# Performance work log

Hardware: AMD Instinct MI355X
Metric: run time of the kernel (lower is better)

Reference implementation:

```python
import jax, jax.numpy as jnp
import numpy as np

B, L, D, H = 2, 2048, 2048, 16
Dh = D // H
THETA = 500000.0


def _init_rope(dim, seq_len, n_heads):
    # Returns freqs_cis of shape (1, seq_len, 1, head_dim//2, 2) -> [..., 0]=cos, [..., 1]=sin
    hd = dim // n_heads
    inv_freqs = 1.0 / (THETA ** (jnp.arange(0, hd, 2, dtype=jnp.float32) / hd))
    t = jnp.arange(seq_len, dtype=jnp.float32)
    freqs = jnp.outer(t, inv_freqs).astype(jnp.float32)  # (L, hd/2)
    fc = jnp.stack([jnp.cos(freqs)[None, :, None, :],
                    jnp.sin(freqs)[None, :, None, :]], axis=3)  # (1, L, 1, 2, hd/2)
    return fc.transpose(0, 1, 2, 4, 3)  # (1, L, 1, hd/2, 2)


def _apply_rope(q, k, freqs_cis):
    def rotate(x):
        x2 = x.reshape(*x.shape[:-1], -1, 2)  # (B, L, H, Dh/2, 2)
        f = freqs_cis[:, :x.shape[1]]
        cos, sin = f[..., 0], f[..., 1]
        r = jnp.stack([x2[..., 0] * cos - x2[..., 1] * sin,
                       x2[..., 1] * cos + x2[..., 0] * sin], axis=-1)
        return r.reshape(*x.shape)
    return rotate(q), rotate(k)


def setup_inputs() -> dict:
    key = jax.random.key(0)
    kx, kq, kk, kv, ko = jax.random.split(key, 5)
    scale = 1.0 / np.sqrt(D)
    x = jax.random.normal(kx, (B, L, D), dtype=jnp.float32)
    Wq = jax.random.normal(kq, (D, H, Dh), dtype=jnp.float32) * scale
    Wk = jax.random.normal(kk, (D, H, Dh), dtype=jnp.float32) * scale
    Wv = jax.random.normal(kv, (D, H, Dh), dtype=jnp.float32) * scale
    Wo = jax.random.normal(ko, (D, D), dtype=jnp.float32) * scale
    return {"x": x, "Wq": Wq, "Wk": Wk, "Wv": Wv, "Wo": Wo}


def reference(x, Wq, Wk, Wv, Wo):
    freqs_cis = _init_rope(D, L, H)
    q = jnp.einsum('bld,dhk->blhk', x, Wq)  # (B, L, H, Dh)
    k = jnp.einsum('bld,dhk->blhk', x, Wk)
    v = jnp.einsum('bld,dhk->blhk', x, Wv)
    q, k = _apply_rope(q, k, freqs_cis)
    q = q / (Dh ** 0.5)
    att = jnp.einsum('bqhd,bkhd->bhqk', q, k)  # (B, H, L, L)
    Lq = x.shape[1]
    mask = jnp.tril(jnp.ones((1, 1, Lq, Lq), dtype=jnp.bool_))
    neg_inf = jnp.finfo(jnp.float32).min
    att = jnp.where(mask, att, neg_inf)
    att = jax.nn.softmax(att, axis=-1)
    out = jnp.einsum('bhqk,bkhd->bqhd', att, v)  # (B, L, H, Dh)
    out = out.reshape(x.shape)
    return jnp.einsum('bld,de->ble', out, Wo)
```

## Files before the change

### kernel.cpp

```cpp
#include <hip/hip_runtime.h>

typedef unsigned short u16;
typedef unsigned int u32;

#define Bb 2
#define Lc 2048
#define Dc 2048
#define Hc 16
#define DhC 128

typedef __bf16 bf16x8 __attribute__((ext_vector_type(8)));
typedef float f32x4 __attribute__((ext_vector_type(4)));
typedef float f32x16 __attribute__((ext_vector_type(16)));

__device__ __forceinline__ u16 f2b(float f) {
  u32 u = __float_as_uint(f);
  u32 r = (u + 0x7fffu + ((u >> 16) & 1u)) >> 16;
  return (u16)r;
}
__device__ __forceinline__ float b2f(u16 u) {
  return __uint_as_float(((u32)u) << 16);
}

__device__ __forceinline__ u32 cvtpk(float lo, float hi) {
  u32 r;
  asm("v_cvt_pk_bf16_f32 %0, %1, %2" : "=v"(r) : "v"(lo), "v"(hi));
  return r;
}

__device__ __forceinline__ void gll16(const void* g, void* l) {
  __builtin_amdgcn_global_load_lds(
      (const __attribute__((address_space(1))) u32*)g,
      (__attribute__((address_space(3))) u32*)l, 16, 0, 0);
}

__global__ __launch_bounds__(256) void sniff_dtype(const u16* __restrict__ x,
                                                   int* __restrict__ flag) {
  __shared__ int bad;
  if (threadIdx.x == 0) bad = 0;
  __syncthreads();
  int local = 0;
  for (int i = threadIdx.x; i < 65536; i += 256) {
    float v = fabsf(b2f(x[i]));
    if (!(v < 1000.f)) local = 1;
  }
  if (local) atomicOr(&bad, 1);
  __syncthreads();
  if (threadIdx.x == 0) *flag = bad;
}

__global__ __launch_bounds__(256) void conv_x(const void* __restrict__ in,
                                              u16* __restrict__ out,
                                              const int* __restrict__ flag) {
  const int f32 = *flag;
  const int i0 = (blockIdx.x * 256 + threadIdx.x) * 4;
  if (f32) {
    const float* p = (const float*)in;
#pragma unroll
    for (int j = 0; j < 4; j++) out[i0 + j] = f2b(p[i0 + j]);
  } else {
    const u16* p = (const u16*)in;
#pragma unroll
    for (int j = 0; j < 4; j++) out[i0 + j] = p[i0 + j];
  }
}

__global__ __launch_bounds__(256) void transpose2d_conv(const void* __restrict__ in,
                                                        u16* __restrict__ out,
                                                        const int* __restrict__ flag) {
  __shared__ __align__(16) u16 tile[64][65];
  const int f32 = *flag;
  const int r0 = blockIdx.y * 64, c0 = blockIdx.x * 64;
  const int tc = threadIdx.x & 63, tr4 = threadIdx.x >> 6;
#pragma unroll
  for (int p = 0; p < 16; p++) {
    int r = tr4 + p * 4;
    size_t idx = (size_t)(r0 + r) * 2048 + c0 + tc;
    tile[r][tc] = f32 ? f2b(((const float*)in)[idx]) : ((const u16*)in)[idx];
  }
  __syncthreads();
#pragma unroll
  for (int p = 0; p < 16; p++) {
    int rr = tr4 + p * 4;
    out[(size_t)(c0 + rr) * 2048 + r0 + tc] = tile[tc][rr];
  }
}

template <typename OutT>
__device__ __forceinline__ void gemmfo_core(const u16* __restrict__ A,
                                            const u16* __restrict__ Bt,
                                            OutT* __restrict__ C,
                                            int Ntiles, size_t bufStride) {
  constexpr int K = 2048;
  constexpr int NTK = K / 32;
  __shared__ __align__(16) u16 Als[4][128 * 32];
  __shared__ __align__(16) u16 Bls[4][256 * 32];

  const int tid = threadIdx.x;
  const int lane = tid & 63, w = tid >> 6;
  const int quad = lane >> 4, l15 = lane & 15;
  const int wm = w >> 2, wn = w & 3;

  const int nwg = 32 * Ntiles;
  const int q8 = nwg >> 3;
  const int id = (int)blockIdx.x;
  const int swz = (id & 7) * q8 + (id >> 3);
  const int m0 = (swz & 31) * 128;
  const int n0 = (swz >> 5) * 256;

  const int sc = (lane >> 4) * 8;
  const u16* aSrc = A + (size_t)(m0 + w * 16 + l15) * K + sc;
  const u16* bSrc0 = Bt + (size_t)(n0 + (2 * w) * 16 + l15) * K + sc;
  const u16* bSrc1 = Bt + (size_t)(n0 + (2 * w + 1) * 16 + l15) * K + sc;

  const f32x4 fz = {0.f, 0.f, 0.f, 0.f};
  f32x4 acc[4][4];
#pragma unroll
  for (int i = 0; i < 4; i++)
#pragma unroll
    for (int j = 0; j < 4; j++) acc[i][j] = fz;

  auto stage = [&](int t) {
    const int s = t & 3;
    const int k = t * 32;
    gll16(aSrc + k, &Als[s][w * 512]);
    gll16(bSrc0 + k, &Bls[s][(2 * w) * 512]);
    gll16(bSrc1 + k, &Bls[s][(2 * w + 1) * 512]);
  };

  auto compute = [&](int t) {
    const u16* abuf = Als[t & 3];
    const u16* bbuf = Bls[t & 3];
    bf16x8 afr[4], bfr[4];
#pragma unroll
    for (int mt = 0; mt < 4; mt++)
      afr[mt] = *(const bf16x8*)(&abuf[(wm * 4 + mt) * 512 + lane * 8]);
#pragma unroll
    for (int nt = 0; nt < 4; nt++)
      bfr[nt] = *(const bf16x8*)(&bbuf[(wn * 4 + nt) * 512 + lane * 8]);
    asm volatile("s_waitcnt lgkmcnt(0)" ::: "memory");
    __builtin_amdgcn_sched_barrier(0);
    __builtin_amdgcn_s_setprio(1);
#pragma unroll
    for (int mt = 0; mt < 4; mt++)
#pragma unroll
      for (int nt = 0; nt < 4; nt++)
        acc[mt][nt] = __builtin_amdgcn_mfma_f32_16x16x32_bf16(
            afr[mt], bfr[nt], acc[mt][nt], 0, 0, 0);
    __builtin_amdgcn_s_setprio(0);
  };

  stage(0); stage(1); stage(2);
  asm volatile("s_waitcnt vmcnt(6)" ::: "memory");
  __builtin_amdgcn_s_barrier();

  for (int t = 0; t < NTK - 3; ++t) {
    stage(t + 3);
    compute(t);
    asm volatile("s_waitcnt vmcnt(6)" ::: "memory");
    __builtin_amdgcn_s_barrier();
  }
  compute(NTK - 3);
  asm volatile("s_waitcnt vmcnt(3)" ::: "memory");
  __builtin_amdgcn_s_barrier();
  compute(NTK - 2);
  asm volatile("s_waitcnt vmcnt(0)" ::: "memory");
  __builtin_amdgcn_s_barrier();
  compute(NTK - 1);

#pragma unroll
  for (int mt = 0; mt < 4; mt++)
#pragma unroll
    for (int nt = 0; nt < 4; nt++) {
      const int colg = n0 + wn * 64 + nt * 16 + l15;
      const size_t cbase = (size_t)(colg >> 11) * bufStride + (colg & 2047);
#pragma unroll
      for (int r = 0; r < 4; r++) {
        const int row = m0 + wm * 64 + mt * 16 + quad * 4 + r;
        const float v = acc[mt][nt][r];
        if constexpr (sizeof(OutT) == 2)
          C[cbase + (size_t)row * 2048] = f2b(v);
        else
          C[cbase + (size_t)row * 2048] = v;
      }
    }
}

__global__ __launch_bounds__(512, 2) void gemmfo_bf(const u16* __restrict__ A,
                                                    const u16* __restrict__ Bt,
                                                    u16* __restrict__ C,
                                                    int Ntiles, size_t bufStride) {
  gemmfo_core<u16>(A, Bt, C, Ntiles, bufStride);
}
__global__ __launch_bounds__(512, 2) void gemmfo_f32(const u16* __restrict__ A,
                                                     const u16* __restrict__ Bt,
                                                     float* __restrict__ C,
                                                     int Ntiles, size_t bufStride) {
  gemmfo_core<float>(A, Bt, C, Ntiles, bufStride);
}

__global__ __launch_bounds__(256) void transpose_v_k(const u16* __restrict__ V,
                                                     u16* __restrict__ Vt) {
  __shared__ __align__(16) u16 tile[64][65];
  const int z = blockIdx.z;
  const int b = z >> 4, h = z & 15;
  const int l0 = blockIdx.y * 64, d0 = blockIdx.x * 64;
  const int tc = threadIdx.x & 63, tr4 = threadIdx.x >> 6;
#pragma unroll
  for (int p = 0; p < 16; p++) {
    int l = tr4 + p * 4;
    tile[l][tc] = V[(size_t)((b * Lc + l0 + l) * Hc + h) * DhC + d0 + tc];
  }
  __syncthreads();
#pragma unroll
  for (int p = 0; p < 16; p++) {
    int dd = tr4 + p * 4;
    Vt[((size_t)z * DhC + d0 + dd) * Lc + l0 + tc] = tile[tc][dd];
  }
}

__global__ __launch_bounds__(256) void rope_qk(u16* __restrict__ Q, u16* __restrict__ K) {
  const int idx = blockIdx.x * 256 + threadIdx.x;
  const int j = idx & 63;
  const int l = (idx >> 10) & 2047;
  const float inv = expf(-0.2050369278f * (float)j);
  const float ang = (float)l * inv;
  float s, c;
  sincosf(ang, &s, &c);
  const size_t off = (size_t)idx * 2;
  const float q0 = b2f(Q[off]), q1 = b2f(Q[off + 1]);
  const float k0 = b2f(K[off]), k1 = b2f(K[off + 1]);
  const float sc = 0.08838834764f;
  Q[off]     = f2b((q0 * c - q1 * s) * sc);
  Q[off + 1] = f2b((q1 * c + q0 * s) * sc);
  K[off]     = f2b(k0 * c - k1 * s);
  K[off + 1] = f2b(k1 * c + k0 * s);
}

#define NEGBIG (-3.0e30f)
__global__ __launch_bounds__(256, 2) void flash_attn(const u16* __restrict__ Q,
                                                     const u16* __restrict__ Kg,
                                                     const u16* __restrict__ Vt,
                                                     u16* __restrict__ O) {
  __shared__ __align__(16) u16 Ks[2][64 * 128];
  __shared__ __align__(16) u16 Vs[2][128 * 64];
  const int tid = threadIdx.x;
  const int lane = tid & 63, w = tid >> 6;
  const int l31 = lane & 31, hib = lane >> 5;
  const int bh = blockIdx.y;
  const int b = bh >> 4, h = bh & 15;
  const int qt = (bh & 16) ? (int)blockIdx.x : (15 - (int)blockIdx.x);
  const int q0 = qt * 128;
  const int qw0 = q0 + w * 32;
  const int nkv = 2 * qt + 2;

  const int krl = lane >> 4, ksl = lane & 15;
  const int vrl = lane >> 3, vsl = lane & 7;

  bf16x8 qf[8];
  {
    const u16* qptr = Q + ((size_t)(b * Lc + qw0 + l31) * Hc + h) * DhC + 8 * hib;
#pragma unroll
    for (int s = 0; s < 8; s++) qf[s] = *(const bf16x8*)(qptr + s * 16);
  }

  {
#pragma unroll
    for (int p = 0; p < 4; p++) {
      const int r = p * 16 + w * 4 + krl;
      const int c = ksl ^ (r & 15);
      gll16(Kg + ((size_t)(b * Lc + r) * Hc + h) * DhC + c * 8,
            &Ks[0][(p * 256 + w * 64) * 8]);
    }
#pragma unroll
    for (int p = 0; p < 4; p++) {
      const int r = p * 32 + w * 8 + vrl;
      const int c = vsl ^ (r & 7);
      gll16(Vt + ((size_t)bh * DhC + r) * Lc + c * 8,
            &Vs[0][(p * 256 + w * 64) * 8]);
    }
  }

  f32x16 o[4];
#pragma unroll
  for (int dt = 0; dt < 4; dt++) o[dt] = (f32x16)0.0f;
  float mrow = NEGBIG, lrow = 0.f;

  __syncthreads();

  for (int kvt = 0; kvt < nkv; kvt++) {
    const int cur = kvt & 1;
    const u16* Ksc = Ks[cur];
    const u16* Vsc = Vs[cur];

    if (kvt + 1 < nkv) {
      const int nv0 = (kvt + 1) * 64;
      const int nxt = cur ^ 1;
#pragma unroll
      for (int p = 0; p < 4; p++) {
        const int r = p * 16 + w * 4 + krl;
        const int c = ksl ^ (r & 15);
        gll16(Kg + ((size_t)(b * Lc + nv0 + r) * Hc + h) * DhC + c * 8,
              &Ks[nxt][(p * 256 + w * 64) * 8]);
      }
#pragma unroll
      for (int p = 0; p < 4; p++) {
        const int r = p * 32 + w * 8 + vrl;
        const int c = vsl ^ (r & 7);
        gll16(Vt + ((size_t)bh * DhC + r) * Lc + nv0 + c * 8,
              &Vs[nxt][(p * 256 + w * 64) * 8]);
      }
    }

    const int kv0 = kvt * 64;
    const bool active = (kv0 <= qw0 + 31);
    if (active) {
      f32x16 s0 = (f32x16)0.0f, s1 = (f32x16)0.0f;
      __builtin_amdgcn_s_setprio(1);
#pragma unroll
      for (int s = 0; s < 8; s++) {
        const int ch = ((2 * s + hib) ^ (l31 & 15)) * 8;
        bf16x8 k0 = *(const bf16x8*)(&Ksc[l31 * 128 + ch]);
        bf16x8 k1 = *(const bf16x8*)(&Ksc[(32 + l31) * 128 + ch]);
        s0 = __builtin_amdgcn_mfma_f32_32x32x16_bf16(k0, qf[s], s0, 0, 0, 0);
        s1 = __builtin_amdgcn_mfma_f32_32x32x16_bf16(k1, qf[s], s1, 0, 0, 0);
      }
      __builtin_amdgcn_s_setprio(0);

      if (kv0 + 63 > qw0) {
        const int qg = qw0 + l31;
#pragma unroll
        for (int r = 0; r < 16; r++) {
          const int cr = (r & 3) + 8 * (r >> 2) + 4 * hib;
          if (kv0 + cr > qg) s0[r] = NEGBIG;
          if (kv0 + 32 + cr > qg) s1[r] = NEGBIG;
        }
      }

      float mx;
      {
        float a[8];
#pragma unroll
        for (int i = 0; i < 8; i++)
          a[i] = fmaxf(fmaxf(s0[i], s0[i + 8]), fmaxf(s1[i], s1[i + 8]));
        float b0 = fmaxf(a[0], a[4]), b1 = fmaxf(a[1], a[5]);
        float b2 = fmaxf(a[2], a[6]), b3 = fmaxf(a[3], a[7]);
        mx = fmaxf(fmaxf(b0, b1), fmaxf(b2, b3));
      }
      mx = fmaxf(mx, __shfl_xor(mx, 32, 64));

      if (!__all(mx - mrow <= 8.f)) {
        const float mnew = fmaxf(mrow, mx);
        const float al = __expf(mrow - mnew);
#pragma unroll
        for (int dt = 0; dt < 4; dt++)
#pragma unroll
          for (int e = 0; e < 16; e++) o[dt][e] *= al;
        lrow *= al;
        mrow = mnew;
      }

#pragma unroll
      for (int i = 0; i < 16; i++) {
        s0[i] = __expf(s0[i] - mrow);
        s1[i] = __expf(s1[i] - mrow);
      }
      float sm;
      {
        float a[8];
#pragma unroll
        for (int i = 0; i < 8; i++)
          a[i] = (s0[i] + s0[i + 8]) + (s1[i] + s1[i + 8]);
        sm = ((a[0] + a[4]) + (a[1] + a[5])) + ((a[2] + a[6]) + (a[3] + a[7]));
      }
      sm += __shfl_xor(sm, 32, 64);
      lrow += sm;

      bf16x8 paf[4];
#pragma unroll
      for (int t = 0; t < 2; t++) {
#pragma unroll
        for (int h8 = 0; h8 < 2; h8++) {
          const int rB = 8 * h8;
          u32 lo0, lo1, hi0, hi1;
          if (t == 0) {
            lo0 = cvtpk(s0[rB + 0], s0[rB + 1]);
            lo1 = cvtpk(s0[rB + 2], s0[rB + 3]);
            hi0 = cvtpk(s0[rB + 4], s0[rB + 5]);
            hi1 = cvtpk(s0[rB + 6], s0[rB + 7]);
          } else {
            lo0 = cvtpk(s1[rB + 0], s1[rB + 1]);
            lo1 = cvtpk(s1[rB + 2], s1[rB + 3]);
            hi0 = cvtpk(s1[rB + 4], s1[rB + 5]);
            hi1 = cvtpk(s1[rB + 6], s1[rB + 7]);
          }
          const u32 g0 = hib ? lo0 : hi0;
          const u32 g1 = hib ? lo1 : hi1;
          const u32 r0 = (u32)__shfl_xor((int)g0, 32, 64);
          const u32 r1 = (u32)__shfl_xor((int)g1, 32, 64);
          union { u32 u[4]; bf16x8 v; } pu;
          pu.u[0] = hib ? r0 : lo0;
          pu.u[1] = hib ? r1 : lo1;
          pu.u[2] = hib ? hi0 : r0;
          pu.u[3] = hib ? hi1 : r1;
          paf[2 * t + h8] = pu.v;
        }
      }

      __builtin_amdgcn_s_setprio(1);
#pragma unroll
      for (int B = 0; B < 4; B++) {
#pragma unroll
        for (int dt = 0; dt < 4; dt++) {
          const bf16x8 vf = *(const bf16x8*)(
              &Vsc[(32 * dt + l31) * 64 + (((2 * B + hib) ^ (l31 & 7))) * 8]);
          o[dt] = __builtin_amdgcn_mfma_f32_32x32x16_bf16(paf[B], vf, o[dt], 0, 0, 0);
        }
      }
      __builtin_amdgcn_s_setprio(0);
    }

    __syncthreads();
  }

#pragma unroll
  for (int r = 0; r < 16; r++) {
    const int cr = (r & 3) + 8 * (r >> 2) + 4 * hib;
    const float linv = 1.0f / __shfl(lrow, cr, 64);
    const size_t rowoff = ((size_t)(b * Lc + qw0 + cr) * Hc + h) * DhC + l31;
#pragma unroll
    for (int dt = 0; dt < 4; dt++)
      O[rowoff + 32 * dt] = f2b(o[dt][r] * linv);
  }
}

extern "C" void kernel_launch(void* const* d_in, const int* in_sizes, int n_in,
                              void* d_out, int out_size, void* d_ws, size_t ws_size,
                              hipStream_t stream) {
  const void* x  = d_in[0];
  const void* Wq = d_in[1];
  const void* Wk = d_in[2];
  const void* Wv = d_in[3];
  const void* Wo = d_in[4];
  float* out = (float*)d_out;

  char* w = (char*)d_ws;
  const size_t WSZ = (size_t)2048 * 2048;
  const size_t XSZ = (size_t)Bb * Lc * Dc;
  int* flag = (int*)w;
  u16* WT  = (u16*)(w + 256);
  u16* xc  = WT + WSZ;
  u16* Qb  = xc + XSZ;
  u16* Kb  = Qb + XSZ;
  u16* Vb  = Kb + XSZ;
  u16* Vtb = xc;
  u16* Ob  = Vb;
  u16* WTall = (u16*)d_out;

  sniff_dtype<<<1, 256, 0, stream>>>((const u16*)x, flag);
  conv_x<<<(int)(XSZ / 1024), 256, 0, stream>>>(x, xc, flag);

  dim3 tgrid(32, 32);

  transpose2d_conv<<<tgrid, 256, 0, stream>>>(Wq, WTall, flag);
  transpose2d_conv<<<tgrid, 256, 0, stream>>>(Wk, WTall + WSZ, flag);
  transpose2d_conv<<<tgrid, 256, 0, stream>>>(Wv, WTall + 2 * WSZ, flag);

  gemmfo_bf<<<dim3(768), 512, 0, stream>>>(xc, WTall, Qb, 24, XSZ);

  rope_qk<<<(Bb * Lc * Hc * 64) / 256, 256, 0, stream>>>(Qb, Kb);

  dim3 vgrid(2, 32, 32);
  transpose_v_k<<<vgrid, 256, 0, stream>>>(Vb, Vtb);

  dim3 fgrid(16, 32);
  flash_attn<<<fgrid, 256, 0, stream>>>(Qb, Kb, Vtb, Ob);

  transpose2d_conv<<<tgrid, 256, 0, stream>>>(Wo, WT, flag);
  gemmfo_f32<<<dim3(256), 512, 0, stream>>>(Ob, WT, out, 8, 0);
}
```

Measured before the change: 614.3 us.

## Shrink GEMM tiles to 128x128, batch weight transposes, and share RoPE trig across batch

The projection GEMMs switch from 512-thread 128x256 tiles with 4-stage LDS buffering to 256-thread 128x128 tiles with 3-stage buffering and four blocks per CU, which doubles the grid and lowers per-block LDS. The three Q/K/V weight transposes merge into one launch. RoPE now computes sincos once per (l, h, j) and applies it to both batch elements, using exp2f. Smaller tiles give more blocks and better occupancy but less operand reuse per block, and a shallower prefetch pipeline.

```diff
diff --git a/kernel.cpp b/kernel.cpp
--- a/kernel.cpp
+++ b/kernel.cpp
@@ -65,11 +65,8 @@
   }
 }
 
-__global__ __launch_bounds__(256) void transpose2d_conv(const void* __restrict__ in,
-                                                        u16* __restrict__ out,
-                                                        const int* __restrict__ flag) {
+__device__ __forceinline__ void tconv_body(const void* in, u16* out, int f32) {
   __shared__ __align__(16) u16 tile[64][65];
-  const int f32 = *flag;
   const int r0 = blockIdx.y * 64, c0 = blockIdx.x * 64;
   const int tc = threadIdx.x & 63, tr4 = threadIdx.x >> 6;
 #pragma unroll
@@ -86,32 +83,48 @@
   }
 }
 
+__global__ __launch_bounds__(256) void transpose2d_conv(const void* __restrict__ in,
+                                                        u16* __restrict__ out,
+                                                        const int* __restrict__ flag) {
+  tconv_body(in, out, *flag);
+}
+
+__global__ __launch_bounds__(256) void transpose3_conv(const void* __restrict__ W0,
+                                                       const void* __restrict__ W1,
+                                                       const void* __restrict__ W2,
+                                                       u16* __restrict__ out,
+                                                       const int* __restrict__ flag) {
+  const int z = blockIdx.z;
+  const void* in = (z == 0) ? W0 : (z == 1) ? W1 : W2;
+  tconv_body(in, out + (size_t)z * 2048 * 2048, *flag);
+}
+
 template <typename OutT>
-__device__ __forceinline__ void gemmfo_core(const u16* __restrict__ A,
-                                            const u16* __restrict__ Bt,
-                                            OutT* __restrict__ C,
-                                            int Ntiles, size_t bufStride) {
+__device__ __forceinline__ void gemmp_core(const u16* __restrict__ A,
+                                           const u16* __restrict__ Bt,
+                                           OutT* __restrict__ C,
+                                           int Ntiles, size_t bufStride) {
   constexpr int K = 2048;
   constexpr int NTK = K / 32;
-  __shared__ __align__(16) u16 Als[4][128 * 32];
-  __shared__ __align__(16) u16 Bls[4][256 * 32];
+  __shared__ __align__(16) u16 Als[3][128 * 32];
+  __shared__ __align__(16) u16 Bls[3][128 * 32];
 
   const int tid = threadIdx.x;
   const int lane = tid & 63, w = tid >> 6;
   const int quad = lane >> 4, l15 = lane & 15;
-  const int wm = w >> 2, wn = w & 3;
+  const int wm = w >> 1, wn = w & 1;
 
   const int nwg = 32 * Ntiles;
   const int q8 = nwg >> 3;
   const int id = (int)blockIdx.x;
   const int swz = (id & 7) * q8 + (id >> 3);
   const int m0 = (swz & 31) * 128;
-  const int n0 = (swz >> 5) * 256;
-
-  const int sc = (lane >> 4) * 8;
-  const u16* aSrc = A + (size_t)(m0 + w * 16 + l15) * K + sc;
-  const u16* bSrc0 = Bt + (size_t)(n0 + (2 * w) * 16 + l15) * K + sc;
-  const u16* bSrc1 = Bt + (size_t)(n0 + (2 * w + 1) * 16 + l15) * K + sc;
+  const int n0 = (swz >> 5) * 128;
+
+  const u16* aSrc0 = A + (size_t)(m0 + (2 * w) * 16 + l15) * K + quad * 8;
+  const u16* aSrc1 = A + (size_t)(m0 + (2 * w + 1) * 16 + l15) * K + quad * 8;
+  const u16* bSrc0 = Bt + (size_t)(n0 + (2 * w) * 16 + l15) * K + quad * 8;
+  const u16* bSrc1 = Bt + (size_t)(n0 + (2 * w + 1) * 16 + l15) * K + quad * 8;
 
   const f32x4 fz = {0.f, 0.f, 0.f, 0.f};
   f32x4 acc[4][4];
@@ -121,23 +134,23 @@
     for (int j = 0; j < 4; j++) acc[i][j] = fz;
 
   auto stage = [&](int t) {
-    const int s = t & 3;
+    const int s = t % 3;
     const int k = t * 32;
-    gll16(aSrc + k, &Als[s][w * 512]);
+    gll16(aSrc0 + k, &Als[s][(2 * w) * 512]);
+    gll16(aSrc1 + k, &Als[s][(2 * w + 1) * 512]);
     gll16(bSrc0 + k, &Bls[s][(2 * w) * 512]);
     gll16(bSrc1 + k, &Bls[s][(2 * w + 1) * 512]);
   };
 
   auto compute = [&](int t) {
-    const u16* abuf = Als[t & 3];
-    const u16* bbuf = Bls[t & 3];
+    const int s = t % 3;
     bf16x8 afr[4], bfr[4];
 #pragma unroll
     for (int mt = 0; mt < 4; mt++)
-      afr[mt] = *(const bf16x8*)(&abuf[(wm * 4 + mt) * 512 + lane * 8]);
+      afr[mt] = *(const bf16x8*)(&Als[s][(wm * 4 + mt) * 512 + lane * 8]);
 #pragma unroll
     for (int nt = 0; nt < 4; nt++)
-      bfr[nt] = *(const bf16x8*)(&bbuf[(wn * 4 + nt) * 512 + lane * 8]);
+      bfr[nt] = *(const bf16x8*)(&Bls[s][(wn * 4 + nt) * 512 + lane * 8]);
     asm volatile("s_waitcnt lgkmcnt(0)" ::: "memory");
     __builtin_amdgcn_sched_barrier(0);
     __builtin_amdgcn_s_setprio(1);
@@ -150,19 +163,17 @@
     __builtin_amdgcn_s_setprio(0);
   };
 
-  stage(0); stage(1); stage(2);
-  asm volatile("s_waitcnt vmcnt(6)" ::: "memory");
+  stage(0);
+  stage(1);
+  asm volatile("s_waitcnt vmcnt(4)" ::: "memory");
   __builtin_amdgcn_s_barrier();
 
-  for (int t = 0; t < NTK - 3; ++t) {
-    stage(t + 3);
+  for (int t = 0; t < NTK - 2; ++t) {
+    stage(t + 2);
     compute(t);
-    asm volatile("s_waitcnt vmcnt(6)" ::: "memory");
+    asm volatile("s_waitcnt vmcnt(4)" ::: "memory");
     __builtin_amdgcn_s_barrier();
   }
-  compute(NTK - 3);
-  asm volatile("s_waitcnt vmcnt(3)" ::: "memory");
-  __builtin_amdgcn_s_barrier();
   compute(NTK - 2);
   asm volatile("s_waitcnt vmcnt(0)" ::: "memory");
   __builtin_amdgcn_s_barrier();
@@ -186,17 +197,17 @@
     }
 }
 
-__global__ __launch_bounds__(512, 2) void gemmfo_bf(const u16* __restrict__ A,
+__global__ __launch_bounds__(256, 4) void gemmp_bf(const u16* __restrict__ A,
+                                                   const u16* __restrict__ Bt,
+                                                   u16* __restrict__ C,
+                                                   int Ntiles, size_t bufStride) {
+  gemmp_core<u16>(A, Bt, C, Ntiles, bufStride);
+}
+__global__ __launch_bounds__(256, 4) void gemmp_f32(const u16* __restrict__ A,
                                                     const u16* __restrict__ Bt,
-                                                    u16* __restrict__ C,
+                                                    float* __restrict__ C,
                                                     int Ntiles, size_t bufStride) {
-  gemmfo_core<u16>(A, Bt, C, Ntiles, bufStride);
-}
-__global__ __launch_bounds__(512, 2) void gemmfo_f32(const u16* __restrict__ A,
-                                                     const u16* __restrict__ Bt,
-                                                     float* __restrict__ C,
-                                                     int Ntiles, size_t bufStride) {
-  gemmfo_core<float>(A, Bt, C, Ntiles, bufStride);
+  gemmp_core<float>(A, Bt, C, Ntiles, bufStride);
 }
 
 __global__ __launch_bounds__(256) void transpose_v_k(const u16* __restrict__ V,
@@ -222,19 +233,23 @@
 __global__ __launch_bounds__(256) void rope_qk(u16* __restrict__ Q, u16* __restrict__ K) {
   const int idx = blockIdx.x * 256 + threadIdx.x;
   const int j = idx & 63;
-  const int l = (idx >> 10) & 2047;
-  const float inv = expf(-0.2050369278f * (float)j);
+  const int h = (idx >> 6) & 15;
+  const int l = idx >> 10;
+  const float inv = exp2f(-0.2958057561f * (float)j);
   const float ang = (float)l * inv;
   float s, c;
   sincosf(ang, &s, &c);
-  const size_t off = (size_t)idx * 2;
-  const float q0 = b2f(Q[off]), q1 = b2f(Q[off + 1]);
-  const float k0 = b2f(K[off]), k1 = b2f(K[off + 1]);
   const float sc = 0.08838834764f;
-  Q[off]     = f2b((q0 * c - q1 * s) * sc);
-  Q[off + 1] = f2b((q1 * c + q0 * s) * sc);
-  K[off]     = f2b(k0 * c - k1 * s);
-  K[off + 1] = f2b(k1 * c + k0 * s);
+#pragma unroll
+  for (int b = 0; b < Bb; b++) {
+    const size_t off = ((size_t)((b * Lc + l) * Hc + h)) * DhC + 2 * j;
+    const float q0 = b2f(Q[off]), q1 = b2f(Q[off + 1]);
+    const float k0 = b2f(K[off]), k1 = b2f(K[off + 1]);
+    Q[off]     = f2b((q0 * c - q1 * s) * sc);
+    Q[off + 1] = f2b((q1 * c + q0 * s) * sc);
+    K[off]     = f2b(k0 * c - k1 * s);
+    K[off + 1] = f2b(k1 * c + k0 * s);
+  }
 }
 
 #define NEGBIG (-3.0e30f)
@@ -460,15 +475,11 @@
   sniff_dtype<<<1, 256, 0, stream>>>((const u16*)x, flag);
   conv_x<<<(int)(XSZ / 1024), 256, 0, stream>>>(x, xc, flag);
 
-  dim3 tgrid(32, 32);
-
-  transpose2d_conv<<<tgrid, 256, 0, stream>>>(Wq, WTall, flag);
-  transpose2d_conv<<<tgrid, 256, 0, stream>>>(Wk, WTall + WSZ, flag);
-  transpose2d_conv<<<tgrid, 256, 0, stream>>>(Wv, WTall + 2 * WSZ, flag);
-
-  gemmfo_bf<<<dim3(768), 512, 0, stream>>>(xc, WTall, Qb, 24, XSZ);
-
-  rope_qk<<<(Bb * Lc * Hc * 64) / 256, 256, 0, stream>>>(Qb, Kb);
+  transpose3_conv<<<dim3(32, 32, 3), 256, 0, stream>>>(Wq, Wk, Wv, WTall, flag);
+
+  gemmp_bf<<<dim3(1536), 256, 0, stream>>>(xc, WTall, Qb, 48, XSZ);
+
+  rope_qk<<<(Lc * Hc * 64) / 256, 256, 0, stream>>>(Qb, Kb);
 
   dim3 vgrid(2, 32, 32);
   transpose_v_k<<<vgrid, 256, 0, stream>>>(Vb, Vtb);
@@ -476,6 +487,7 @@
   dim3 fgrid(16, 32);
   flash_attn<<<fgrid, 256, 0, stream>>>(Qb, Kb, Vtb, Ob);
 
+  dim3 tgrid(32, 32);
   transpose2d_conv<<<tgrid, 256, 0, stream>>>(Wo, WT, flag);
-  gemmfo_f32<<<dim3(256), 512, 0, stream>>>(Ob, WT, out, 8, 0);
-}
+  gemmp_f32<<<dim3(512), 256, 0, stream>>>(Ob, WT, out, 16, 0);
+}
```

Result: faster. 572.1 us (-6.9%).
